# Optimization experiments

Measured on AMD Instinct MI355X. Metric: run time of the kernel, lower is better.

Reference implementation:

```python
import math
import jax, jax.numpy as jnp
import numpy as np

COLORS = 10
MAX_SHIFT = 5
B, H, W = 32, 128, 128

_shifts = [(dy, dx) for dy in range(-MAX_SHIFT, MAX_SHIFT + 1)
           for dx in range(-MAX_SHIFT, MAX_SHIFT + 1)
           if not (dy == 0 and dx == 0)]  # include_identity=False
DYS = jnp.asarray(np.array([s[0] for s in _shifts], dtype=np.int32))
DXS = jnp.asarray(np.array([s[1] for s in _shifts], dtype=np.int32))


def _shift_all(grid):
    """Apply every (dy,dx) shift to an int grid [B,H,W] with zero padding.

    out[s, b, y, x] = grid[b, y-dy_s, x-dx_s] if in-bounds else 0,
    exactly matching apply_shift_batch (uncovered regions are color 0).
    Returns [S, B, H, W].
    """
    b, h, w = grid.shape
    padded = jnp.pad(grid, ((0, 0), (MAX_SHIFT, MAX_SHIFT), (MAX_SHIFT, MAX_SHIFT)))
    def one(dy, dx):
        return jax.lax.dynamic_slice(padded, (0, MAX_SHIFT - dy, MAX_SHIFT - dx), (b, h, w))
    return jax.vmap(one)(DYS, DXS)


def setup_inputs() -> dict:
    key = jax.random.key(0)
    k1, k2, k3 = jax.random.split(key, 3)
    return {
        "demo_in": jax.random.randint(k1, (B, H, W), 0, COLORS, dtype=jnp.int32),
        "demo_out": jax.random.randint(k2, (B, H, W), 0, COLORS, dtype=jnp.int32),
        "query_in": jax.random.randint(k3, (B, H, W), 0, COLORS, dtype=jnp.int32),
        "color_log_weight": jnp.zeros((COLORS,), dtype=jnp.float32),
        "logit_scale": jnp.asarray(4.0, dtype=jnp.float32),
    }


def reference(demo_in, demo_out, query_in, color_log_weight, logit_scale):
    b, h, w = query_in.shape
    S = DYS.shape[0]

    # Per-shift correlation score. one_hot(shifted)*one_hot(demo_out)*w summed
    # over (C,H,W) == sum over pixels of w[demo_out] * (shifted == demo_out).
    shifted_demo = _shift_all(demo_in)                       # [S,B,H,W] int
    w_out = jnp.exp(color_log_weight)[demo_out]              # [B,H,W]
    eq = (shifted_demo == demo_out[None]).astype(jnp.float32)
    match = jnp.sum(eq * w_out[None], axis=(2, 3))           # [S,B]
    scale = jnp.minimum(jnp.exp(logit_scale), 100.0)
    scores = match.T / math.sqrt(h * w) * scale              # [B,S]
    attention = jax.nn.softmax(scores, axis=1)               # [B,S]

    # Weighted accumulation of one-hot shifted queries, done as a scatter-add
    # into the color channel (avoids materializing [S,B,C,H,W]).
    shifted_query = _shift_all(query_in)                     # [S,B,H,W] int
    b_idx = jnp.arange(b)[None, :, None, None]
    y_idx = jnp.arange(h)[None, None, :, None]
    x_idx = jnp.arange(w)[None, None, None, :]
    attn_b = jnp.broadcast_to(attention.T[:, :, None, None], (S, b, h, w))
    accum = jnp.zeros((b, COLORS, h, w), dtype=jnp.float32)
    accum = accum.at[b_idx, shifted_query, y_idx, x_idx].add(attn_b)
    return jnp.log(jnp.maximum(accum, 1e-6))
```

## Files before the change

kernel.cpp:

```cpp
#include <hip/hip_runtime.h>
#include <hip/hip_bf16.h>
#include <math.h>

#define COLORS 10
#define NB 32
#define H 128
#define W 128
#define NS 120
#define HW (H*W)
#define STRIPS 8
#define SH 16
#define DROWS 26
#define DINW 8

typedef unsigned int u32;
typedef unsigned long long u64;
typedef float f32x4 __attribute__((ext_vector_type(4)));
typedef short bf16x8 __attribute__((ext_vector_type(8)));

__global__ __launch_bounds__(256) void match_strip(
    const int* __restrict__ demo_in, const int* __restrict__ demo_out,
    const float* __restrict__ clw, float* __restrict__ mpart)
{
    __shared__ u32 din_p[COLORS][DROWS][DINW];
    __shared__ u32 dout_p[COLORS][SH][4];
    __shared__ float wexp[COLORS];
    __shared__ float pp[128];

    int t = threadIdx.x;
    int strip = blockIdx.x;
    int b = blockIdx.y;
    int wave = t >> 6, lane = t & 63;

    if (t < COLORS) wexp[t] = __expf(clw[t]);

    const int* di = demo_in  + b * HW;
    const int* dd = demo_out + b * HW;
    int y0 = strip * SH;

    for (int r = wave; r < DROWS; r += 4) {
        int gy = y0 - 5 + r;
        bool ok = (gy >= 0 && gy < H);
        int v0 = 0, v1 = 0;
        if (ok) { v0 = di[gy * W + lane]; v1 = di[gy * W + 64 + lane]; }
        #pragma unroll
        for (int c = 0; c < COLORS; c++) {
            u64 h0 = __ballot(v0 == c);
            u64 h1 = __ballot(v1 == c);
            u64 P0, P1, P2;
            if (!ok) {
                P0 = (c == 0) ? ~0ull : 0ull;
                P1 = P0;
                P2 = (c == 0) ? 0x3FFull : 0ull;
            } else {
                u64 lm = (c == 0) ? 0x1Full  : 0ull;
                u64 rm = (c == 0) ? 0x3E0ull : 0ull;
                P0 = (h0 << 5) | lm;
                P1 = (h0 >> 59) | (h1 << 5);
                P2 = (h1 >> 59) | rm;
            }
            if (lane == 0) {
                u32* w = &din_p[c][r][0];
                w[0] = (u32)P0; w[1] = (u32)(P0 >> 32);
                w[2] = (u32)P1; w[3] = (u32)(P1 >> 32);
                w[4] = (u32)P2; w[5] = 0; w[6] = 0; w[7] = 0;
            }
        }
    }
    for (int r = wave; r < SH; r += 4) {
        int gy = y0 + r;
        int v0 = dd[gy * W + lane], v1 = dd[gy * W + 64 + lane];
        #pragma unroll
        for (int c = 0; c < COLORS; c++) {
            u64 h0 = __ballot(v0 == c);
            u64 h1 = __ballot(v1 == c);
            if (lane == 0) {
                u32* w = &dout_p[c][r][0];
                w[0] = (u32)h0; w[1] = (u32)(h0 >> 32);
                w[2] = (u32)h1; w[3] = (u32)(h1 >> 32);
            }
        }
    }
    __syncthreads();

    int s  = t & 127;
    int yh = t >> 7;
    float acc = 0.f;
    if (s < NS) {
        int lin = s + (s >= 60);
        int dy = lin / 11 - 5, dx = lin % 11 - 5;
        int k = 5 - dx;
        for (int c = 0; c < COLORS; c++) {
            int cnt = 0;
            #pragma unroll
            for (int yy = 0; yy < 8; yy++) {
                int y = yh * 8 + yy;
                int r = y - dy + 5;
                const u32* dr   = &din_p[c][r][0];
                const u32* orow = &dout_p[c][y][0];
                u32 s0 = __builtin_amdgcn_alignbit(dr[1], dr[0], k);
                u32 s1 = __builtin_amdgcn_alignbit(dr[2], dr[1], k);
                u32 s2 = __builtin_amdgcn_alignbit(dr[3], dr[2], k);
                u32 s3 = __builtin_amdgcn_alignbit(dr[4], dr[3], k);
                cnt += __popc(s0 & orow[0]) + __popc(s1 & orow[1])
                     + __popc(s2 & orow[2]) + __popc(s3 & orow[3]);
            }
            acc += wexp[c] * (float)cnt;
        }
    }
    if (yh == 1) pp[s] = acc;
    __syncthreads();
    if (yh == 0 && s < NS)
        mpart[(b * NS + s) * STRIPS + strip] = acc + pp[s];
}

__global__ __launch_bounds__(256) void accum_fused(
    const int* __restrict__ query_in, const float* __restrict__ mpart,
    const float* __restrict__ logit_scale, float* __restrict__ out)
{
    __shared__ __align__(16) int qs[14][144];
    __shared__ float sm[NS];
    __shared__ unsigned short abf[128];

    int t  = threadIdx.x;
    int y0 = blockIdx.x * 4;
    int b  = blockIdx.y;
    const int* q = query_in + b * HW;

    int vstage[8];
    #pragma unroll
    for (int i = 0; i < 8; i++) {
        int idx = t + i * 256;
        int r = idx / 144;
        int p = idx - r * 144;
        int gy = y0 - 5 + r;
        bool ok = (idx < 2016) & (gy >= 0) & (gy < H) & (p >= 5) & (p < 133);
        int cy = gy < 0 ? 0 : (gy > 127 ? 127 : gy);
        int cx = p < 5 ? 0 : (p > 132 ? 127 : p - 5);
        int ld = q[cy * W + cx];
        vstage[i] = ok ? ld : 0;
    }

    float scale = fminf(__expf(logit_scale[0]), 100.0f) * (1.0f / 128.0f);
    if (t < NS) {
        const float* mp = mpart + (t + b * NS) * STRIPS;
        float4 v0 = *reinterpret_cast<const float4*>(mp);
        float4 v1 = *reinterpret_cast<const float4*>(mp + 4);
        sm[t] = (v0.x + v0.y + v0.z + v0.w + v1.x + v1.y + v1.z + v1.w) * scale;
    }
    __syncthreads();
    if (t < 64) {
        float s0 = sm[t];
        float s1 = (t + 64 < NS) ? sm[t + 64] : -INFINITY;
        float m = fmaxf(s0, s1);
        for (int off = 32; off > 0; off >>= 1) m = fmaxf(m, __shfl_xor(m, off, 64));
        float e0 = __expf(s0 - m);
        float e1 = (t + 64 < NS) ? __expf(s1 - m) : 0.f;
        float sum = e0 + e1;
        for (int off = 32; off > 0; off >>= 1) sum += __shfl_xor(sum, off, 64);
        float inv = 1.0f / sum;
        sm[t] = e0 * inv;
        if (t + 64 < NS) sm[t + 64] = e1 * inv;
    }
    __syncthreads();
    if (t < 128) {
        unsigned short v = 0;
        if (t < 121 && t != 60) {
            int si = t - (t > 60);
            __hip_bfloat16 hb = __float2bfloat16(sm[si]);
            v = *reinterpret_cast<unsigned short*>(&hb);
        }
        abf[t] = v;
    }

    #pragma unroll
    for (int i = 0; i < 8; i++) {
        int idx = t + i * 256;
        if (idx < 2016) ((int*)qs)[idx] = vstage[i];
    }
    __syncthreads();

    int lane = t & 63, wv = t >> 6;
    int mrow = lane & 15, g8 = (lane >> 4) * 8;
    uint4 afr[11];
    #pragma unroll
    for (int st = 0; st < 11; st++) {
        u32 wq[4];
        #pragma unroll
        for (int p = 0; p < 4; p++) {
            int j0 = mrow + 10 - (g8 + p * 2);
            int j1 = j0 - 1;
            int i0 = (j0 >= 0 && j0 <= 10) ? (10 - st) * 11 + j0 : 121;
            int i1 = (j1 >= 0 && j1 <= 10) ? (10 - st) * 11 + j1 : 121;
            wq[p] = (u32)abf[i0] | ((u32)abf[i1] << 16);
        }
        afr[st] = make_uint4(wq[0], wq[1], wq[2], wq[3]);
    }

    int c = lane & 15, g = lane >> 4;

    #pragma unroll
    for (int ti = 0; ti < 2; ti++) {
        int x0 = wv * 32 + ti * 16;

        uint4 bf[14];
        #pragma unroll
        for (int r = 0; r < 14; r++) {
            uint4 qa = *reinterpret_cast<const uint4*>(&qs[r][x0 + 8 * g]);
            uint4 qb = *reinterpret_cast<const uint4*>(&qs[r][x0 + 8 * g + 4]);
            u32 b0 = ((int)qa.x == c ? 0x3F80u : 0u) | ((int)qa.y == c ? 0x3F800000u : 0u);
            u32 b1 = ((int)qa.z == c ? 0x3F80u : 0u) | ((int)qa.w == c ? 0x3F800000u : 0u);
            u32 b2 = ((int)qb.x == c ? 0x3F80u : 0u) | ((int)qb.y == c ? 0x3F800000u : 0u);
            u32 b3 = ((int)qb.z == c ? 0x3F80u : 0u) | ((int)qb.w == c ? 0x3F800000u : 0u);
            bf[r] = make_uint4(b0, b1, b2, b3);
        }

        f32x4 acc[4];
        #pragma unroll
        for (int j = 0; j < 4; j++) acc[j] = (f32x4){0.f, 0.f, 0.f, 0.f};

        #pragma unroll
        for (int st = 0; st < 11; st++) {
            #pragma unroll
            for (int j = 0; j < 4; j++) {
                union { uint4 u; bf16x8 v; } A, B;
                A.u = afr[st];
                B.u = bf[st + j];
                acc[j] = __builtin_amdgcn_mfma_f32_16x16x32_bf16(A.v, B.v, acc[j], 0, 0, 0);
            }
        }

        if (c < COLORS) {
            #pragma unroll
            for (int j = 0; j < 4; j++) {
                float* ob = out + (((size_t)b * COLORS + c) * H + (y0 + j)) * W + x0 + 4 * g;
                float4 rr;
                rr.x = __logf(fmaxf(acc[j][0], 1e-6f));
                rr.y = __logf(fmaxf(acc[j][1], 1e-6f));
                rr.z = __logf(fmaxf(acc[j][2], 1e-6f));
                rr.w = __logf(fmaxf(acc[j][3], 1e-6f));
                *reinterpret_cast<float4*>(ob) = rr;
            }
        }
    }
}

__global__ __launch_bounds__(256) void match_kernel(
    const int* __restrict__ demo_in, const int* __restrict__ demo_out,
    const float* __restrict__ clw, float* __restrict__ match)
{
    int blk = blockIdx.x;
    int b = blk / NS;
    int s = blk % NS;
    int lin = s + (s >= 60 ? 1 : 0);
    int dy = lin / 11 - 5, dx = lin % 11 - 5;

    __shared__ float wexp[COLORS];
    int tid = threadIdx.x;
    if (tid < COLORS) wexp[tid] = expf(clw[tid]);
    __syncthreads();

    const int* __restrict__ din  = demo_in  + b * HW;
    const int* __restrict__ dout = demo_out + b * HW;

    float partial = 0.f;
    for (int i = tid; i < HW; i += 256) {
        int yy = i >> 7, xx = i & 127;
        int co = dout[i];
        int sy = yy - dy, sx = xx - dx;
        int v = 0;
        if (sy >= 0 && sy < H && sx >= 0 && sx < W) v = din[sy * W + sx];
        if (v == co) partial += wexp[co];
    }
    for (int off = 32; off > 0; off >>= 1) partial += __shfl_down(partial, off, 64);
    __shared__ float wsum[4];
    if ((tid & 63) == 0) wsum[tid >> 6] = partial;
    __syncthreads();
    if (tid == 0) match[blk] = wsum[0] + wsum[1] + wsum[2] + wsum[3];
}

__global__ __launch_bounds__(64) void softmax_kernel(
    const float* __restrict__ match, const float* __restrict__ logit_scale,
    float* __restrict__ attention)
{
    int b = blockIdx.x;
    int lane = threadIdx.x;
    float scale = fminf(expf(logit_scale[0]), 100.0f) / sqrtf((float)HW);
    int i0 = lane, i1 = lane + 64;
    float s0 = match[b * NS + i0] * scale;
    float s1 = (i1 < NS) ? match[b * NS + i1] * scale : -INFINITY;
    float m = fmaxf(s0, s1);
    for (int off = 32; off > 0; off >>= 1) m = fmaxf(m, __shfl_xor(m, off, 64));
    float e0 = expf(s0 - m);
    float e1 = (i1 < NS) ? expf(s1 - m) : 0.f;
    float sum = e0 + e1;
    for (int off = 32; off > 0; off >>= 1) sum += __shfl_xor(sum, off, 64);
    float inv = 1.0f / sum;
    attention[b * NS + i0] = e0 * inv;
    if (i1 < NS) attention[b * NS + i1] = e1 * inv;
}

__global__ __launch_bounds__(128) void accum_kernel(
    const int* __restrict__ query_in, const float* __restrict__ attention,
    float* __restrict__ out)
{
    int blk = blockIdx.x;
    int b = blk >> 7;
    int y = blk & 127;
    int x = threadIdx.x;

    __shared__ float att[NS];
    if (threadIdx.x < NS) att[threadIdx.x] = attention[b * NS + threadIdx.x];
    __syncthreads();

    const int* __restrict__ q = query_in + b * HW;
    float acc[COLORS];
    #pragma unroll
    for (int c = 0; c < COLORS; c++) acc[c] = 0.f;

    #pragma unroll 4
    for (int s = 0; s < NS; s++) {
        int lin = s + (s >= 60 ? 1 : 0);
        int dy = lin / 11 - 5, dx = lin % 11 - 5;
        int sy = y - dy, sx = x - dx;
        int v = 0;
        if (sy >= 0 && sy < H && sx >= 0 && sx < W) v = q[sy * W + sx];
        float a = att[s];
        #pragma unroll
        for (int c = 0; c < COLORS; c++) acc[c] += (v == c) ? a : 0.f;
    }
    float* __restrict__ ob = out + (size_t)b * COLORS * HW + y * W + x;
    #pragma unroll
    for (int c = 0; c < COLORS; c++) ob[c * HW] = __logf(fmaxf(acc[c], 1e-6f));
}

extern "C" void kernel_launch(void* const* d_in, const int* in_sizes, int n_in,
                              void* d_out, int out_size, void* d_ws, size_t ws_size,
                              hipStream_t stream) {
    const int*   demo_in     = (const int*)d_in[0];
    const int*   demo_out    = (const int*)d_in[1];
    const int*   query_in    = (const int*)d_in[2];
    const float* clw         = (const float*)d_in[3];
    const float* logit_scale = (const float*)d_in[4];
    float* out = (float*)d_out;

    size_t needed = (size_t)NB * NS * STRIPS * sizeof(float);

    if (ws_size >= needed) {
        float* mpart = (float*)d_ws;
        match_strip<<<dim3(STRIPS, NB), 256, 0, stream>>>(demo_in, demo_out, clw, mpart);
        accum_fused<<<dim3(H / 4, NB), 256, 0, stream>>>(query_in, mpart, logit_scale, out);
    } else {
        float* match = (float*)d_ws;
        float* att   = match + NB * NS;
        match_kernel<<<NB * NS, 256, 0, stream>>>(demo_in, demo_out, clw, match);
        softmax_kernel<<<NB, 64, 0, stream>>>(match, logit_scale, att);
        accum_kernel<<<NB * H, 128, 0, stream>>>(query_in, att, out);
    }
}
```

Measured before the change: 35.35 us.

## Widen blocks to 512 threads, pack query tile as bytes, share A fragments

The match kernel now runs 512 threads, with each shift split across four lanes that are reduced by shuffles instead of a shared-memory partial sum. The accumulate kernel processes 8 output rows per block, halving the blocks per batch. It stores the padded query tile as bytes rather than ints to shrink LDS, and builds the bf16 attention MFMA fragments once in shared memory instead of per thread. This cuts redundant halo loads and per-thread fragment construction, at the cost of fewer blocks and byte-unpacking ALU work.

```diff
diff --git a/kernel.cpp b/kernel.cpp
--- a/kernel.cpp
+++ b/kernel.cpp
@@ -13,19 +13,19 @@
 #define DROWS 26
 #define DINW 8
 
+typedef unsigned char u8;
 typedef unsigned int u32;
 typedef unsigned long long u64;
 typedef float f32x4 __attribute__((ext_vector_type(4)));
 typedef short bf16x8 __attribute__((ext_vector_type(8)));
 
-__global__ __launch_bounds__(256) void match_strip(
+__global__ __launch_bounds__(512) void match_strip(
     const int* __restrict__ demo_in, const int* __restrict__ demo_out,
     const float* __restrict__ clw, float* __restrict__ mpart)
 {
     __shared__ u32 din_p[COLORS][DROWS][DINW];
     __shared__ u32 dout_p[COLORS][SH][4];
     __shared__ float wexp[COLORS];
-    __shared__ float pp[128];
 
     int t = threadIdx.x;
     int strip = blockIdx.x;
@@ -38,7 +38,7 @@
     const int* dd = demo_out + b * HW;
     int y0 = strip * SH;
 
-    for (int r = wave; r < DROWS; r += 4) {
+    for (int r = wave; r < DROWS; r += 8) {
         int gy = y0 - 5 + r;
         bool ok = (gy >= 0 && gy < H);
         int v0 = 0, v1 = 0;
@@ -67,7 +67,7 @@
             }
         }
     }
-    for (int r = wave; r < SH; r += 4) {
+    for (int r = wave; r < SH; r += 8) {
         int gy = y0 + r;
         int v0 = dd[gy * W + lane], v1 = dd[gy * W + 64 + lane];
         #pragma unroll
@@ -83,18 +83,17 @@
     }
     __syncthreads();
 
-    int s  = t & 127;
-    int yh = t >> 7;
+    int s = t >> 2, q = t & 3;
     float acc = 0.f;
-    if (s < NS) {
+    if (t < 4 * NS) {
         int lin = s + (s >= 60);
         int dy = lin / 11 - 5, dx = lin % 11 - 5;
         int k = 5 - dx;
         for (int c = 0; c < COLORS; c++) {
             int cnt = 0;
             #pragma unroll
-            for (int yy = 0; yy < 8; yy++) {
-                int y = yh * 8 + yy;
+            for (int yy = 0; yy < 4; yy++) {
+                int y = q * 4 + yy;
                 int r = y - dy + 5;
                 const u32* dr   = &din_p[c][r][0];
                 const u32* orow = &dout_p[c][y][0];
@@ -108,37 +107,55 @@
             acc += wexp[c] * (float)cnt;
         }
     }
-    if (yh == 1) pp[s] = acc;
-    __syncthreads();
-    if (yh == 0 && s < NS)
-        mpart[(b * NS + s) * STRIPS + strip] = acc + pp[s];
-}
-
-__global__ __launch_bounds__(256) void accum_fused(
+    acc += __shfl_down(acc, 1, 64);
+    acc += __shfl_down(acc, 2, 64);
+    if (q == 0 && t < 4 * NS)
+        mpart[(b * NS + s) * STRIPS + strip] = acc;
+}
+
+#define AR 18
+__global__ __launch_bounds__(512) void accum_fused(
     const int* __restrict__ query_in, const float* __restrict__ mpart,
     const float* __restrict__ logit_scale, float* __restrict__ out)
 {
-    __shared__ __align__(16) int qs[14][144];
+    __shared__ u8  qs[AR][144];
     __shared__ float sm[NS];
     __shared__ unsigned short abf[128];
+    __shared__ __align__(16) u32 Agl[11][64][4];
 
     int t  = threadIdx.x;
-    int y0 = blockIdx.x * 4;
+    int y0 = blockIdx.x * 8;
     int b  = blockIdx.y;
     const int* q = query_in + b * HW;
 
-    int vstage[8];
-    #pragma unroll
-    for (int i = 0; i < 8; i++) {
-        int idx = t + i * 256;
-        int r = idx / 144;
-        int p = idx - r * 144;
-        int gy = y0 - 5 + r;
-        bool ok = (idx < 2016) & (gy >= 0) & (gy < H) & (p >= 5) & (p < 133);
-        int cy = gy < 0 ? 0 : (gy > 127 ? 127 : gy);
-        int cx = p < 5 ? 0 : (p > 132 ? 127 : p - 5);
-        int ld = q[cy * W + cx];
-        vstage[i] = ok ? ld : 0;
+    u32 pk0 = 0, pk1 = 0;
+    {
+        int g = t;
+        #pragma unroll
+        for (int e = 0; e < 4; e++) {
+            int idx = g * 4 + e;
+            int r = idx / 144, p = idx - r * 144;
+            int gy = y0 - 5 + r;
+            bool ok = (gy >= 0) & (gy < H) & (p >= 5) & (p < 133);
+            int cy = gy < 0 ? 0 : (gy > 127 ? 127 : gy);
+            int cx = p < 5 ? 0 : (p > 132 ? 127 : p - 5);
+            int v = q[cy * W + cx];
+            pk0 |= (u32)(ok ? v : 0) << (8 * e);
+        }
+    }
+    if (t < 648 - 512) {
+        int g = t + 512;
+        #pragma unroll
+        for (int e = 0; e < 4; e++) {
+            int idx = g * 4 + e;
+            int r = idx / 144, p = idx - r * 144;
+            int gy = y0 - 5 + r;
+            bool ok = (gy >= 0) & (gy < H) & (p >= 5) & (p < 133);
+            int cy = gy < 0 ? 0 : (gy > 127 ? 127 : gy);
+            int cx = p < 5 ? 0 : (p > 132 ? 127 : p - 5);
+            int v = q[cy * W + cx];
+            pk1 |= (u32)(ok ? v : 0) << (8 * e);
+        }
     }
 
     float scale = fminf(__expf(logit_scale[0]), 100.0f) * (1.0f / 128.0f);
@@ -148,7 +165,11 @@
         float4 v1 = *reinterpret_cast<const float4*>(mp + 4);
         sm[t] = (v0.x + v0.y + v0.z + v0.w + v1.x + v1.y + v1.z + v1.w) * scale;
     }
-    __syncthreads();
+
+    ((u32*)qs)[t] = pk0;
+    if (t < 648 - 512) ((u32*)qs)[t + 512] = pk1;
+    __syncthreads();
+
     if (t < 64) {
         float s0 = sm[t];
         float s1 = (t + 64 < NS) ? sm[t + 64] : -INFINITY;
@@ -172,46 +193,63 @@
         }
         abf[t] = v;
     }
-
-    #pragma unroll
-    for (int i = 0; i < 8; i++) {
-        int idx = t + i * 256;
-        if (idx < 2016) ((int*)qs)[idx] = vstage[i];
-    }
-    __syncthreads();
-
-    int lane = t & 63, wv = t >> 6;
-    int mrow = lane & 15, g8 = (lane >> 4) * 8;
-    uint4 afr[11];
-    #pragma unroll
-    for (int st = 0; st < 11; st++) {
-        u32 wq[4];
+    __syncthreads();
+
+    {
+        int e = t;
+        int st = e >> 6, l = e & 63;
+        int mrow = l & 15, g8 = (l >> 4) * 8;
         #pragma unroll
         for (int p = 0; p < 4; p++) {
             int j0 = mrow + 10 - (g8 + p * 2);
             int j1 = j0 - 1;
             int i0 = (j0 >= 0 && j0 <= 10) ? (10 - st) * 11 + j0 : 121;
             int i1 = (j1 >= 0 && j1 <= 10) ? (10 - st) * 11 + j1 : 121;
-            wq[p] = (u32)abf[i0] | ((u32)abf[i1] << 16);
-        }
-        afr[st] = make_uint4(wq[0], wq[1], wq[2], wq[3]);
-    }
-
+            Agl[st][l][p] = (u32)abf[i0] | ((u32)abf[i1] << 16);
+        }
+    }
+    if (t < 704 - 512) {
+        int e = t + 512;
+        int st = e >> 6, l = e & 63;
+        int mrow = l & 15, g8 = (l >> 4) * 8;
+        #pragma unroll
+        for (int p = 0; p < 4; p++) {
+            int j0 = mrow + 10 - (g8 + p * 2);
+            int j1 = j0 - 1;
+            int i0 = (j0 >= 0 && j0 <= 10) ? (10 - st) * 11 + j0 : 121;
+            int i1 = (j1 >= 0 && j1 <= 10) ? (10 - st) * 11 + j1 : 121;
+            Agl[st][l][p] = (u32)abf[i0] | ((u32)abf[i1] << 16);
+        }
+    }
+    __syncthreads();
+
+    int lane = t & 63, w = t >> 6;
+    uint4 afr[11];
+    #pragma unroll
+    for (int st = 0; st < 11; st++)
+        afr[st] = *reinterpret_cast<const uint4*>(&Agl[st][lane][0]);
+
+    int jb = (w >> 2) * 4;
+    int xq = w & 3;
     int c = lane & 15, g = lane >> 4;
 
     #pragma unroll
     for (int ti = 0; ti < 2; ti++) {
-        int x0 = wv * 32 + ti * 16;
+        int x0 = xq * 32 + ti * 16;
 
         uint4 bf[14];
         #pragma unroll
         for (int r = 0; r < 14; r++) {
-            uint4 qa = *reinterpret_cast<const uint4*>(&qs[r][x0 + 8 * g]);
-            uint4 qb = *reinterpret_cast<const uint4*>(&qs[r][x0 + 8 * g + 4]);
-            u32 b0 = ((int)qa.x == c ? 0x3F80u : 0u) | ((int)qa.y == c ? 0x3F800000u : 0u);
-            u32 b1 = ((int)qa.z == c ? 0x3F80u : 0u) | ((int)qa.w == c ? 0x3F800000u : 0u);
-            u32 b2 = ((int)qb.x == c ? 0x3F80u : 0u) | ((int)qb.y == c ? 0x3F800000u : 0u);
-            u32 b3 = ((int)qb.z == c ? 0x3F80u : 0u) | ((int)qb.w == c ? 0x3F800000u : 0u);
+            u64 eight = *reinterpret_cast<const u64*>(&qs[jb + r][x0 + 8 * g]);
+            u32 lo = (u32)eight, hi = (u32)(eight >> 32);
+            u32 b0 = ((int)(lo & 255) == c ? 0x3F80u : 0u)
+                   | ((int)((lo >> 8)  & 255) == c ? 0x3F800000u : 0u);
+            u32 b1 = ((int)((lo >> 16) & 255) == c ? 0x3F80u : 0u)
+                   | ((int)((lo >> 24) & 255) == c ? 0x3F800000u : 0u);
+            u32 b2 = ((int)(hi & 255) == c ? 0x3F80u : 0u)
+                   | ((int)((hi >> 8)  & 255) == c ? 0x3F800000u : 0u);
+            u32 b3 = ((int)((hi >> 16) & 255) == c ? 0x3F80u : 0u)
+                   | ((int)((hi >> 24) & 255) == c ? 0x3F800000u : 0u);
             bf[r] = make_uint4(b0, b1, b2, b3);
         }
 
@@ -233,7 +271,7 @@
         if (c < COLORS) {
             #pragma unroll
             for (int j = 0; j < 4; j++) {
-                float* ob = out + (((size_t)b * COLORS + c) * H + (y0 + j)) * W + x0 + 4 * g;
+                float* ob = out + (((size_t)b * COLORS + c) * H + (y0 + jb + j)) * W + x0 + 4 * g;
                 float4 rr;
                 rr.x = __logf(fmaxf(acc[j][0], 1e-6f));
                 rr.y = __logf(fmaxf(acc[j][1], 1e-6f));
@@ -348,8 +386,8 @@
 
     if (ws_size >= needed) {
         float* mpart = (float*)d_ws;
-        match_strip<<<dim3(STRIPS, NB), 256, 0, stream>>>(demo_in, demo_out, clw, mpart);
-        accum_fused<<<dim3(H / 4, NB), 256, 0, stream>>>(query_in, mpart, logit_scale, out);
+        match_strip<<<dim3(STRIPS, NB), 512, 0, stream>>>(demo_in, demo_out, clw, mpart);
+        accum_fused<<<dim3(H / 8, NB), 512, 0, stream>>>(query_in, mpart, logit_scale, out);
     } else {
         float* match = (float*)d_ws;
         float* att   = match + NB * NS;
```

After: 29.82 us. -15.6%, faster.
